# Performance work log

Hardware: AMD Instinct MI355X
Metric: run time of the kernel (lower is better)

## Reference

```python
import jax, jax.numpy as jnp
import numpy as np

N = 50000      # nodes
E = 640000     # edges
F_IN = 128     # input features
H = 128        # hidden = 2**7
C = 40         # classes


def setup_inputs() -> dict:
    key = jax.random.key(0)
    ks = jax.random.split(key, 10)
    x = jax.random.normal(ks[0], (N, F_IN), dtype=jnp.float32)
    edge_index = jax.random.randint(ks[1], (2, E), 0, N, dtype=jnp.int32)
    edge_weight = jax.random.uniform(ks[2], (E,), dtype=jnp.float32)
    def glorot(k, fan_in, fan_out):
        s = (6.0 / (fan_in + fan_out)) ** 0.5
        return jax.random.uniform(k, (fan_in, fan_out), jnp.float32, -s, s)
    return {
        "x": x,
        "edge_index": edge_index,
        "edge_weight": edge_weight,
        "W1": glorot(ks[3], F_IN, H), "b1": jnp.zeros((H,), jnp.float32),
        "W2": glorot(ks[4], H, H),    "b2": jnp.zeros((H,), jnp.float32),
        "W3": glorot(ks[5], H, C),    "b3": jnp.zeros((C,), jnp.float32),
    }


def gcn_conv(x, W, b, src, dst, ew, n):
    """PyG GCNConv: add self-loops, symmetric deg normalization, gather-scatter-add."""
    loop = jnp.arange(n, dtype=src.dtype)
    src_sl = jnp.concatenate([src, loop])
    dst_sl = jnp.concatenate([dst, loop])
    w_sl = jnp.concatenate([ew, jnp.ones((n,), ew.dtype)])
    deg = jax.ops.segment_sum(w_sl, dst_sl, num_segments=n)         # [N]
    dinv = jnp.where(deg > 0, jax.lax.rsqrt(deg), 0.0)
    norm = dinv[src_sl] * w_sl * dinv[dst_sl]                        # [E+N]
    h = x @ W                                                        # [N, out]
    msg = h[src_sl] * norm[:, None]                                  # gather + scale
    out = jax.ops.segment_sum(msg, dst_sl, num_segments=n)          # scatter-add
    return out + b


def reference(x, edge_index, edge_weight, W1, b1, W2, b2, W3, b3):
    # eval-mode forward: dropout and dropedge are identity (training=False)
    src, dst = edge_index[0], edge_index[1]
    n = x.shape[0]
    h = jax.nn.relu(gcn_conv(x, W1, b1, src, dst, edge_weight, n))
    h = jax.nn.relu(gcn_conv(h, W2, b2, src, dst, edge_weight, n))
    return gcn_conv(h, W3, b3, src, dst, edge_weight, n)
```

## Files before the change

### kernel.cpp

```cpp
#include <hip/hip_runtime.h>
#include <hip/hip_fp16.h>

constexpr int N_NODES = 50000;
constexpr int N_EDGES = 640000;

constexpr int NBLK  = 256;
constexpr int EPB   = N_EDGES / NBLK;
constexpr int NBUCK = (N_NODES + 255) / 256;
constexpr int GBM   = (N_NODES + 63) / 64;

typedef _Float16 half8  __attribute__((ext_vector_type(8)));
typedef _Float16 half4v __attribute__((ext_vector_type(4)));
typedef float    floatx4 __attribute__((ext_vector_type(4)));


__global__ void wconv_k(const float* __restrict__ W1, const float* __restrict__ W2,
                        const float* __restrict__ W3, _Float16* __restrict__ Wt1,
                        _Float16* __restrict__ Wt2, _Float16* __restrict__ Wt3) {
    int i = blockIdx.x * 256 + threadIdx.x;
    if (i < 16384) {
        int n = i >> 7, k = i & 127;
        Wt1[n * 128 + k] = (_Float16)W1[k * 128 + n];
    } else if (i < 32768) {
        int j = i - 16384; int n = j >> 7, k = j & 127;
        Wt2[n * 128 + k] = (_Float16)W2[k * 128 + n];
    } else if (i < 32768 + 6144) {
        int j = i - 32768; int n = j >> 7, k = j & 127;
        Wt3[n * 128 + k] = (_Float16)((n < 40) ? W3[k * 40 + n] : 0.f);
    }
}


template<typename TIN, int F_OUT, int NT, bool FUSE_HIST>
__global__ __launch_bounds__(256) void gemm_mfma_k(const TIN* __restrict__ X,
        const _Float16* __restrict__ Wt, __half* __restrict__ H,
        const int* __restrict__ dst, int* __restrict__ gh) {
    if constexpr (FUSE_HIST) {
        if (blockIdx.x < NBLK) {
            __shared__ int lh[256];
            int t = threadIdx.x, b = blockIdx.x;
            lh[t] = 0;
            __syncthreads();
            int e0 = b * EPB;
            for (int j = t; j < EPB; j += 256)
                atomicAdd(&lh[dst[e0 + j] >> 8], 1);
            __syncthreads();
            if (t < NBUCK) gh[b * NBUCK + t] = lh[t];
            return;
        }
    }
    int bid = FUSE_HIST ? (int)blockIdx.x - NBLK : (int)blockIdx.x;

    __shared__ _Float16 Xs[64 * 136];
    int tid = threadIdx.x;
    int row0 = bid * 64;

    if constexpr (sizeof(TIN) == 4) {
        for (int idx = tid; idx < 2048; idx += 256) {
            int r = idx >> 5, c4 = idx & 31;
            float4 v = {0.f, 0.f, 0.f, 0.f};
            if (row0 + r < N_NODES)
                v = *(const float4*)((const float*)X + (size_t)(row0 + r) * 128 + c4 * 4);
            half4v h;
            h[0] = (_Float16)v.x; h[1] = (_Float16)v.y;
            h[2] = (_Float16)v.z; h[3] = (_Float16)v.w;
            *(half4v*)&Xs[r * 136 + c4 * 4] = h;
        }
    } else {
        for (int idx = tid; idx < 1024; idx += 256) {
            int r = idx >> 4, c8 = idx & 15;
            int4 v = {0, 0, 0, 0};
            if (row0 + r < N_NODES)
                v = *(const int4*)((const __half*)X + (size_t)(row0 + r) * 128 + c8 * 8);
            *(int4*)&Xs[r * 136 + c8 * 8] = v;
        }
    }
    __syncthreads();

    int lane = tid & 63;
    int wv   = tid >> 6;
    int m    = lane & 15;
    int q    = lane >> 4;

    half8 af[4];
    #pragma unroll
    for (int kt = 0; kt < 4; kt++)
        af[kt] = *(const half8*)&Xs[(wv * 16 + m) * 136 + kt * 32 + q * 8];

    floatx4 acc[NT];
    #pragma unroll
    for (int nt = 0; nt < NT; nt++) { acc[nt][0] = 0.f; acc[nt][1] = 0.f; acc[nt][2] = 0.f; acc[nt][3] = 0.f; }

    #pragma unroll
    for (int nt = 0; nt < NT; nt++) {
        const _Float16* wp = Wt + (size_t)(nt * 16 + m) * 128 + q * 8;
        half8 b0 = *(const half8*)(wp);
        half8 b1 = *(const half8*)(wp + 32);
        half8 b2 = *(const half8*)(wp + 64);
        half8 b3 = *(const half8*)(wp + 96);
        acc[nt] = __builtin_amdgcn_mfma_f32_16x16x32_f16(af[0], b0, acc[nt], 0, 0, 0);
        acc[nt] = __builtin_amdgcn_mfma_f32_16x16x32_f16(af[1], b1, acc[nt], 0, 0, 0);
        acc[nt] = __builtin_amdgcn_mfma_f32_16x16x32_f16(af[2], b2, acc[nt], 0, 0, 0);
        acc[nt] = __builtin_amdgcn_mfma_f32_16x16x32_f16(af[3], b3, acc[nt], 0, 0, 0);
    }

    #pragma unroll
    for (int nt = 0; nt < NT; nt++) {
        #pragma unroll
        for (int r = 0; r < 4; r++)
            Xs[(wv * 16 + q * 4 + r) * 136 + nt * 16 + m] = (_Float16)acc[nt][r];
    }

    if constexpr (F_OUT == 128) {
        for (int g = lane; g < 256; g += 64) {
            int r = g >> 4, c8 = g & 15;
            int row = row0 + wv * 16 + r;
            if (row < N_NODES)
                *(int4*)((__half*)H + (size_t)row * 128 + c8 * 8) =
                    *(const int4*)&Xs[(wv * 16 + r) * 136 + c8 * 8];
        }
    } else {
        for (int g = lane; g < 80; g += 64) {
            int r = g / 5, seg = g - r * 5;
            int row = row0 + wv * 16 + r;
            if (row < N_NODES)
                *(int4*)((__half*)H + (size_t)row * 40 + seg * 8) =
                    *(const int4*)&Xs[(wv * 16 + r) * 136 + seg * 8];
        }
    }
}


__global__ __launch_bounds__(256) void scan1_k(int* __restrict__ gh, int* __restrict__ total) {
    __shared__ int s[256];
    int t = threadIdx.x, b = blockIdx.x;
    int v = gh[t * NBUCK + b];
    s[t] = v;
    __syncthreads();
    int x = v;
    for (int off = 1; off < 256; off <<= 1) {
        int u = (t >= off) ? s[t - off] : 0;
        __syncthreads();
        x += u; s[t] = x;
        __syncthreads();
    }
    gh[t * NBUCK + b] = x - v;
    if (t == 255) total[b] = x;
}


__global__ __launch_bounds__(256) void bucket_k(const int* __restrict__ src,
        const int* __restrict__ dst, const float* __restrict__ ew,
        const int* __restrict__ gh, const int* __restrict__ total,
        int2* __restrict__ bkt) {
    __shared__ int cur[256];
    __shared__ int sc[256];
    int t = threadIdx.x, b = blockIdx.x;
    int v = (t < NBUCK) ? total[t] : 0;
    sc[t] = v;
    __syncthreads();
    int x = v;
    for (int off = 1; off < 256; off <<= 1) {
        int u = (t >= off) ? sc[t - off] : 0;
        __syncthreads();
        x += u; sc[t] = x;
        __syncthreads();
    }
    if (t < NBUCK) cur[t] = (x - v) + gh[b * NBUCK + t];
    __syncthreads();
    int e0 = b * EPB;
    for (int j = t; j < EPB; j += 256) {
        int d = dst[e0 + j];
        int pos = atomicAdd(&cur[d >> 8], 1);
        bkt[pos] = make_int2(src[e0 + j] | (d << 16), __float_as_int(ew[e0 + j]));
    }
}


__global__ __launch_bounds__(256) void final_k(const int2* __restrict__ bkt,
        const int* __restrict__ total, int2* __restrict__ ev,
        int* __restrict__ rowptr, float* __restrict__ dinv) {
    __shared__ int   cnt[256];
    __shared__ float wsum[256];
    __shared__ int   s[256];
    int t = threadIdx.x, b = blockIdx.x;

    cnt[t] = 0; wsum[t] = 0.f;

    int v = (t < NBUCK) ? total[t] : 0;
    s[t] = v;
    __syncthreads();
    int x = v;
    for (int off = 1; off < 256; off <<= 1) {
        int u = (t >= off) ? s[t - off] : 0;
        __syncthreads();
        x += u; s[t] = x;
        __syncthreads();
    }
    int base = (b == 0) ? 0 : s[b - 1];
    int cntb = total[b];
    __syncthreads();

    for (int j = t; j < cntb; j += 256) {
        int2 r = bkt[base + j];
        int bin = (r.x >> 16) & 255;
        atomicAdd(&cnt[bin], 1);
        atomicAdd(&wsum[bin], __int_as_float(r.y));
    }
    __syncthreads();

    int v2 = cnt[t];
    s[t] = v2;
    __syncthreads();
    int x2 = v2;
    for (int off = 1; off < 256; off <<= 1) {
        int u = (t >= off) ? s[t - off] : 0;
        __syncthreads();
        x2 += u; s[t] = x2;
        __syncthreads();
    }
    int off_t = x2 - v2;
    int nd = b * 256 + t;
    float dv = rsqrtf(1.0f + wsum[t]);
    if (nd < N_NODES) {
        rowptr[nd] = base + off_t;
        dinv[nd]   = dv;
    }
    if (b == 0 && t == 0) rowptr[N_NODES] = N_EDGES;
    wsum[t] = dv;
    s[t] = off_t;
    __syncthreads();

    for (int j = t; j < cntb; j += 256) {
        int2 r = bkt[base + j];
        int bin  = (r.x >> 16) & 255;
        int sidx = r.x & 0xFFFF;
        float wv = __int_as_float(r.y) * wsum[bin];
        int p = atomicAdd(&s[bin], 1);
        ev[base + p] = make_int2(sidx, __float_as_int(wv));
    }
}


template<bool PREMUL>
__global__ __launch_bounds__(256) void agg128_k(const __half* __restrict__ H,
        int2* __restrict__ ev, const int* __restrict__ rowptr,
        const float* __restrict__ dinv, const float* __restrict__ bias,
        __half* __restrict__ out) {
    int lane = threadIdx.x & 63;
    int node = __builtin_amdgcn_readfirstlane(blockIdx.x * 4 + (threadIdx.x >> 6));
    if (node >= N_NODES) return;
    const __half2* __restrict__ H2 = (const __half2*)H;
    float di = dinv[node];
    float dii = di * di;
    float2 hs = __half22float2(H2[(size_t)node * 64 + lane]);
    float ax = dii * hs.x, ay = dii * hs.y;
    int e0 = rowptr[node], e1 = rowptr[node + 1];
    int e = e0;
    for (; e + 4 <= e1; e += 4) {
        int2 p0 = ev[e + 0];
        int2 p1 = ev[e + 1];
        int2 p2 = ev[e + 2];
        int2 p3 = ev[e + 3];
        float v0 = __int_as_float(p0.y);
        float v1 = __int_as_float(p1.y);
        float v2 = __int_as_float(p2.y);
        float v3 = __int_as_float(p3.y);
        if constexpr (PREMUL) {
            v0 *= dinv[p0.x]; v1 *= dinv[p1.x];
            v2 *= dinv[p2.x]; v3 *= dinv[p3.x];
            if (lane == 0) {
                ev[e + 0].y = __float_as_int(v0);
                ev[e + 1].y = __float_as_int(v1);
                ev[e + 2].y = __float_as_int(v2);
                ev[e + 3].y = __float_as_int(v3);
            }
        }
        float2 g0 = __half22float2(H2[(size_t)p0.x * 64 + lane]);
        float2 g1 = __half22float2(H2[(size_t)p1.x * 64 + lane]);
        float2 g2 = __half22float2(H2[(size_t)p2.x * 64 + lane]);
        float2 g3 = __half22float2(H2[(size_t)p3.x * 64 + lane]);
        ax = fmaf(v0, g0.x, ax); ay = fmaf(v0, g0.y, ay);
        ax = fmaf(v1, g1.x, ax); ay = fmaf(v1, g1.y, ay);
        ax = fmaf(v2, g2.x, ax); ay = fmaf(v2, g2.y, ay);
        ax = fmaf(v3, g3.x, ax); ay = fmaf(v3, g3.y, ay);
    }
    for (; e < e1; e++) {
        int2 p = ev[e];
        float v = __int_as_float(p.y);
        if constexpr (PREMUL) {
            v *= dinv[p.x];
            if (lane == 0) ev[e].y = __float_as_int(v);
        }
        float2 g = __half22float2(H2[(size_t)p.x * 64 + lane]);
        ax = fmaf(v, g.x, ax);
        ay = fmaf(v, g.y, ay);
    }
    float2 b = *(const float2*)&bias[2 * lane];
    ax = fmaxf(ax + b.x, 0.f);
    ay = fmaxf(ay + b.y, 0.f);
    ((__half2*)out)[(size_t)node * 64 + lane] = __float22half2_rn(make_float2(ax, ay));
}


__global__ __launch_bounds__(256) void agg40_k(const __half* __restrict__ Y,
        const int2* __restrict__ ev, const int* __restrict__ rowptr,
        const float* __restrict__ dinv, const float* __restrict__ bias,
        float* __restrict__ out) {
    int lane = threadIdx.x & 63;
    int node = __builtin_amdgcn_readfirstlane(blockIdx.x * 4 + (threadIdx.x >> 6));
    if (node >= N_NODES) return;
    const __half2* __restrict__ Y2 = (const __half2*)Y;
    int h = lane >> 5;
    int l = lane & 31;
    int f = (l < 20) ? l : 0;
    float di = dinv[node];
    float dii = di * di;
    float ax = 0.f, ay = 0.f;
    if (h == 0) {
        float2 ys = __half22float2(Y2[(size_t)node * 20 + f]);
        ax = dii * ys.x; ay = dii * ys.y;
    }
    int e0 = rowptr[node], e1 = rowptr[node + 1];
    int e = e0;
    for (; e + 4 <= e1; e += 4) {
        int2 p0 = ev[e + h * 2 + 0];
        int2 p1 = ev[e + h * 2 + 1];
        float2 g0 = __half22float2(Y2[(size_t)p0.x * 20 + f]);
        float2 g1 = __half22float2(Y2[(size_t)p1.x * 20 + f]);
        float v0 = __int_as_float(p0.y);
        float v1 = __int_as_float(p1.y);
        ax = fmaf(v0, g0.x, ax); ay = fmaf(v0, g0.y, ay);
        ax = fmaf(v1, g1.x, ax); ay = fmaf(v1, g1.y, ay);
    }
    for (int ee = e + h; ee < e1; ee += 2) {
        int2 p = ev[ee];
        float v = __int_as_float(p.y);
        float2 g = __half22float2(Y2[(size_t)p.x * 20 + f]);
        ax = fmaf(v, g.x, ax);
        ay = fmaf(v, g.y, ay);
    }
    ax += __shfl_xor(ax, 32);
    ay += __shfl_xor(ay, 32);
    if (lane < 20) {
        float2 b = *(const float2*)&bias[2 * lane];
        float2 o;
        o.x = ax + b.x;
        o.y = ay + b.y;
        *(float2*)&out[(size_t)node * 40 + 2 * lane] = o;
    }
}


extern "C" void kernel_launch(void* const* d_in, const int* in_sizes, int n_in,
                              void* d_out, int out_size, void* d_ws, size_t ws_size,
                              hipStream_t stream) {
    const float* x  = (const float*)d_in[0];
    const int*   ei = (const int*)d_in[1];
    const int*   src = ei;
    const int*   dst = ei + N_EDGES;
    const float* ew = (const float*)d_in[2];
    const float* W1 = (const float*)d_in[3];
    const float* b1 = (const float*)d_in[4];
    const float* W2 = (const float*)d_in[5];
    const float* b2 = (const float*)d_in[6];
    const float* W3 = (const float*)d_in[7];
    const float* b3 = (const float*)d_in[8];
    float* out = (float*)d_out;

    char* w = (char*)d_ws;
    auto alloc = [&](size_t bytes) {
        char* p = w;
        w += (bytes + 255) & ~(size_t)255;
        return p;
    };
    float*     dinv   = (float*)    alloc((size_t)N_NODES * 4);
    int*       rowptr = (int*)      alloc((size_t)(N_NODES + 1) * 4);
    int*       gh     = (int*)      alloc((size_t)NBLK * NBUCK * 4);
    int*       total  = (int*)      alloc((size_t)NBUCK * 4);
    int2*      bkt    = (int2*)     alloc((size_t)N_EDGES * 8);
    int2*      ev     = (int2*)     alloc((size_t)N_EDGES * 8);
    __half*    hbuf   = (__half*)   alloc((size_t)N_NODES * 128 * 2);
    __half*    abuf   = (__half*)   alloc((size_t)N_NODES * 128 * 2);
    __half*    ybuf   = (__half*)   alloc((size_t)N_NODES * 40 * 2);
    _Float16*  Wt1    = (_Float16*) alloc((size_t)128 * 128 * 2);
    _Float16*  Wt2    = (_Float16*) alloc((size_t)128 * 128 * 2);
    _Float16*  Wt3    = (_Float16*) alloc((size_t)48 * 128 * 2);

    constexpr int GA = (N_NODES + 3) / 4;

    wconv_k<<<152, 256, 0, stream>>>(W1, W2, W3, Wt1, Wt2, Wt3);
    gemm_mfma_k<float, 128, 8, true><<<NBLK + GBM, 256, 0, stream>>>(x, Wt1, hbuf, dst, gh);
    scan1_k<<<NBUCK, 256, 0, stream>>>(gh, total);
    bucket_k<<<NBLK, 256, 0, stream>>>(src, dst, ew, gh, total, bkt);
    final_k<<<NBUCK, 256, 0, stream>>>(bkt, total, ev, rowptr, dinv);

    agg128_k<true ><<<GA, 256, 0, stream>>>(hbuf, ev, rowptr, dinv, b1, abuf);
    gemm_mfma_k<__half, 128, 8, false><<<GBM, 256, 0, stream>>>(abuf, Wt2, hbuf, nullptr, nullptr);
    agg128_k<false><<<GA, 256, 0, stream>>>(hbuf, ev, rowptr, dinv, b2, abuf);
    gemm_mfma_k<__half, 40, 3, false><<<GBM, 256, 0, stream>>>(abuf, Wt3, ybuf, nullptr, nullptr);
    agg40_k<<<GA, 256, 0, stream>>>(ybuf, ev, rowptr, dinv, b3, out);
}
```

Baseline: 257.0 us.

## Fuse neighbor aggregation with following MFMA GEMM in one kernel per layer

Replaces the separate aggregation and GEMM kernels for layers 1→2 and 2→3 with one fused kernel. Each 512-thread block aggregates 64 nodes into shared memory, then runs the MFMA projection from there. This removes the global round-trip of the aggregated activations and one kernel launch per layer. In exchange, each wave serially walks 8 nodes' edge lists, so gather parallelism and latency hiding per block drop, grid size falls from ~12.5k to ~782 blocks, and the GEMM phase waits on the slowest node's edges.

After: 244.5 us. 1.05x faster.

```diff
diff --git a/kernel.cpp b/kernel.cpp
--- a/kernel.cpp
+++ b/kernel.cpp
@@ -111,22 +111,12 @@
             Xs[(wv * 16 + q * 4 + r) * 136 + nt * 16 + m] = (_Float16)acc[nt][r];
     }
 
-    if constexpr (F_OUT == 128) {
-        for (int g = lane; g < 256; g += 64) {
-            int r = g >> 4, c8 = g & 15;
-            int row = row0 + wv * 16 + r;
-            if (row < N_NODES)
-                *(int4*)((__half*)H + (size_t)row * 128 + c8 * 8) =
-                    *(const int4*)&Xs[(wv * 16 + r) * 136 + c8 * 8];
-        }
-    } else {
-        for (int g = lane; g < 80; g += 64) {
-            int r = g / 5, seg = g - r * 5;
-            int row = row0 + wv * 16 + r;
-            if (row < N_NODES)
-                *(int4*)((__half*)H + (size_t)row * 40 + seg * 8) =
-                    *(const int4*)&Xs[(wv * 16 + r) * 136 + seg * 8];
-        }
+    for (int g = lane; g < 256; g += 64) {
+        int r = g >> 4, c8 = g & 15;
+        int row = row0 + wv * 16 + r;
+        if (row < N_NODES)
+            *(int4*)((__half*)H + (size_t)row * 128 + c8 * 8) =
+                *(const int4*)&Xs[(wv * 16 + r) * 136 + c8 * 8];
     }
 }
 
@@ -242,64 +232,136 @@
 }
 
 
-template<bool PREMUL>
-__global__ __launch_bounds__(256) void agg128_k(const __half* __restrict__ H,
+template<int F_OUT, int NT, bool PREMUL>
+__global__ __launch_bounds__(512) void aggemm_k(const __half* __restrict__ Hin,
         int2* __restrict__ ev, const int* __restrict__ rowptr,
         const float* __restrict__ dinv, const float* __restrict__ bias,
-        __half* __restrict__ out) {
-    int lane = threadIdx.x & 63;
-    int node = __builtin_amdgcn_readfirstlane(blockIdx.x * 4 + (threadIdx.x >> 6));
-    if (node >= N_NODES) return;
-    const __half2* __restrict__ H2 = (const __half2*)H;
-    float di = dinv[node];
-    float dii = di * di;
-    float2 hs = __half22float2(H2[(size_t)node * 64 + lane]);
-    float ax = dii * hs.x, ay = dii * hs.y;
-    int e0 = rowptr[node], e1 = rowptr[node + 1];
-    int e = e0;
-    for (; e + 4 <= e1; e += 4) {
-        int2 p0 = ev[e + 0];
-        int2 p1 = ev[e + 1];
-        int2 p2 = ev[e + 2];
-        int2 p3 = ev[e + 3];
-        float v0 = __int_as_float(p0.y);
-        float v1 = __int_as_float(p1.y);
-        float v2 = __int_as_float(p2.y);
-        float v3 = __int_as_float(p3.y);
-        if constexpr (PREMUL) {
-            v0 *= dinv[p0.x]; v1 *= dinv[p1.x];
-            v2 *= dinv[p2.x]; v3 *= dinv[p3.x];
-            if (lane == 0) {
-                ev[e + 0].y = __float_as_int(v0);
-                ev[e + 1].y = __float_as_int(v1);
-                ev[e + 2].y = __float_as_int(v2);
-                ev[e + 3].y = __float_as_int(v3);
+        const _Float16* __restrict__ Wt, __half* __restrict__ Hout) {
+    __shared__ _Float16 Xs[64 * 136];
+    int tid  = threadIdx.x;
+    int lane = tid & 63;
+    int wv   = tid >> 6;
+    int row0 = (int)blockIdx.x * 64;
+    const __half2* __restrict__ H2 = (const __half2*)Hin;
+    float2 bb = *(const float2*)&bias[2 * lane];
+
+    for (int r = 0; r < 8; ++r) {
+        int lrow = wv * 8 + r;
+        int node = __builtin_amdgcn_readfirstlane(row0 + lrow);
+        float ax = 0.f, ay = 0.f;
+        if (node < N_NODES) {
+            float di  = dinv[node];
+            float dii = di * di;
+            float2 hs = __half22float2(H2[(size_t)node * 64 + lane]);
+            ax = dii * hs.x; ay = dii * hs.y;
+            int e0 = rowptr[node], e1 = rowptr[node + 1];
+            int e = e0;
+            for (; e + 4 <= e1; e += 4) {
+                int2 p0 = ev[e + 0];
+                int2 p1 = ev[e + 1];
+                int2 p2 = ev[e + 2];
+                int2 p3 = ev[e + 3];
+                float v0 = __int_as_float(p0.y);
+                float v1 = __int_as_float(p1.y);
+                float v2 = __int_as_float(p2.y);
+                float v3 = __int_as_float(p3.y);
+                if constexpr (PREMUL) {
+                    v0 *= dinv[p0.x]; v1 *= dinv[p1.x];
+                    v2 *= dinv[p2.x]; v3 *= dinv[p3.x];
+                    if (lane == 0) {
+                        ev[e + 0].y = __float_as_int(v0);
+                        ev[e + 1].y = __float_as_int(v1);
+                        ev[e + 2].y = __float_as_int(v2);
+                        ev[e + 3].y = __float_as_int(v3);
+                    }
+                }
+                float2 g0 = __half22float2(H2[(size_t)p0.x * 64 + lane]);
+                float2 g1 = __half22float2(H2[(size_t)p1.x * 64 + lane]);
+                float2 g2 = __half22float2(H2[(size_t)p2.x * 64 + lane]);
+                float2 g3 = __half22float2(H2[(size_t)p3.x * 64 + lane]);
+                ax = fmaf(v0, g0.x, ax); ay = fmaf(v0, g0.y, ay);
+                ax = fmaf(v1, g1.x, ax); ay = fmaf(v1, g1.y, ay);
+                ax = fmaf(v2, g2.x, ax); ay = fmaf(v2, g2.y, ay);
+                ax = fmaf(v3, g3.x, ax); ay = fmaf(v3, g3.y, ay);
             }
-        }
-        float2 g0 = __half22float2(H2[(size_t)p0.x * 64 + lane]);
-        float2 g1 = __half22float2(H2[(size_t)p1.x * 64 + lane]);
-        float2 g2 = __half22float2(H2[(size_t)p2.x * 64 + lane]);
-        float2 g3 = __half22float2(H2[(size_t)p3.x * 64 + lane]);
-        ax = fmaf(v0, g0.x, ax); ay = fmaf(v0, g0.y, ay);
-        ax = fmaf(v1, g1.x, ax); ay = fmaf(v1, g1.y, ay);
-        ax = fmaf(v2, g2.x, ax); ay = fmaf(v2, g2.y, ay);
-        ax = fmaf(v3, g3.x, ax); ay = fmaf(v3, g3.y, ay);
-    }
-    for (; e < e1; e++) {
-        int2 p = ev[e];
-        float v = __int_as_float(p.y);
-        if constexpr (PREMUL) {
-            v *= dinv[p.x];
-            if (lane == 0) ev[e].y = __float_as_int(v);
-        }
-        float2 g = __half22float2(H2[(size_t)p.x * 64 + lane]);
-        ax = fmaf(v, g.x, ax);
-        ay = fmaf(v, g.y, ay);
-    }
-    float2 b = *(const float2*)&bias[2 * lane];
-    ax = fmaxf(ax + b.x, 0.f);
-    ay = fmaxf(ay + b.y, 0.f);
-    ((__half2*)out)[(size_t)node * 64 + lane] = __float22half2_rn(make_float2(ax, ay));
+            for (; e < e1; e++) {
+                int2 p = ev[e];
+                float v = __int_as_float(p.y);
+                if constexpr (PREMUL) {
+                    v *= dinv[p.x];
+                    if (lane == 0) ev[e].y = __float_as_int(v);
+                }
+                float2 g = __half22float2(H2[(size_t)p.x * 64 + lane]);
+                ax = fmaf(v, g.x, ax);
+                ay = fmaf(v, g.y, ay);
+            }
+            ax = fmaxf(ax + bb.x, 0.f);
+            ay = fmaxf(ay + bb.y, 0.f);
+        }
+        ((__half2*)&Xs[lrow * 136])[lane] = __float22half2_rn(make_float2(ax, ay));
+    }
+    __syncthreads();
+
+    int rg = wv & 3;
+    int ch = wv >> 2;
+    int m  = lane & 15;
+    int q  = lane >> 4;
+
+    half8 af[4];
+    #pragma unroll
+    for (int kt = 0; kt < 4; kt++)
+        af[kt] = *(const half8*)&Xs[(rg * 16 + m) * 136 + kt * 32 + q * 8];
+    __syncthreads();
+
+    constexpr int NACC = (NT + 1) / 2;
+    floatx4 acc[NACC];
+    #pragma unroll
+    for (int i = 0; i < NACC; i++) { acc[i][0] = 0.f; acc[i][1] = 0.f; acc[i][2] = 0.f; acc[i][3] = 0.f; }
+
+    #pragma unroll
+    for (int i = 0; i < NACC; i++) {
+        int nt = ch + 2 * i;
+        if (nt < NT) {
+            const _Float16* wp = Wt + (size_t)(nt * 16 + m) * 128 + q * 8;
+            half8 b0 = *(const half8*)(wp);
+            half8 b1 = *(const half8*)(wp + 32);
+            half8 b2 = *(const half8*)(wp + 64);
+            half8 b3 = *(const half8*)(wp + 96);
+            acc[i] = __builtin_amdgcn_mfma_f32_16x16x32_f16(af[0], b0, acc[i], 0, 0, 0);
+            acc[i] = __builtin_amdgcn_mfma_f32_16x16x32_f16(af[1], b1, acc[i], 0, 0, 0);
+            acc[i] = __builtin_amdgcn_mfma_f32_16x16x32_f16(af[2], b2, acc[i], 0, 0, 0);
+            acc[i] = __builtin_amdgcn_mfma_f32_16x16x32_f16(af[3], b3, acc[i], 0, 0, 0);
+        }
+    }
+
+    #pragma unroll
+    for (int i = 0; i < NACC; i++) {
+        int nt = ch + 2 * i;
+        if (nt < NT) {
+            #pragma unroll
+            for (int rr = 0; rr < 4; rr++)
+                Xs[(rg * 16 + q * 4 + rr) * 136 + nt * 16 + m] = (_Float16)acc[i][rr];
+        }
+    }
+    __syncthreads();
+
+    if constexpr (F_OUT == 128) {
+        for (int g = lane; g < 128; g += 64) {
+            int rr = g >> 3, c8 = (g & 7) + ch * 8;
+            int row = row0 + rg * 16 + rr;
+            if (row < N_NODES)
+                *(int4*)((__half*)Hout + (size_t)row * 128 + c8 * 8) =
+                    *(const int4*)&Xs[(rg * 16 + rr) * 136 + c8 * 8];
+        }
+    } else {
+        for (int g = lane + ch * 40; g < 40 + ch * 40; g += 64) {
+            int rr = g / 5, seg = g - rr * 5;
+            int row = row0 + rg * 16 + rr;
+            if (row < N_NODES)
+                *(int4*)((__half*)Hout + (size_t)row * 40 + seg * 8) =
+                    *(const int4*)&Xs[(rg * 16 + rr) * 136 + seg * 8];
+        }
+    }
 }
 
 
@@ -395,9 +457,7 @@
     bucket_k<<<NBLK, 256, 0, stream>>>(src, dst, ew, gh, total, bkt);
     final_k<<<NBUCK, 256, 0, stream>>>(bkt, total, ev, rowptr, dinv);
 
-    agg128_k<true ><<<GA, 256, 0, stream>>>(hbuf, ev, rowptr, dinv, b1, abuf);
-    gemm_mfma_k<__half, 128, 8, false><<<GBM, 256, 0, stream>>>(abuf, Wt2, hbuf, nullptr, nullptr);
-    agg128_k<false><<<GA, 256, 0, stream>>>(hbuf, ev, rowptr, dinv, b2, abuf);
-    gemm_mfma_k<__half, 40, 3, false><<<GBM, 256, 0, stream>>>(abuf, Wt3, ybuf, nullptr, nullptr);
+    aggemm_k<128, 8, true ><<<GBM, 512, 0, stream>>>(hbuf, ev, rowptr, dinv, b1, Wt2, abuf);
+    aggemm_k<40,  3, false><<<GBM, 512, 0, stream>>>(abuf, ev, rowptr, dinv, b2, Wt3, ybuf);
     agg40_k<<<GA, 256, 0, stream>>>(ybuf, ev, rowptr, dinv, b3, out);
 }
```
